# Kernel tuning notes

Hardware: AMD Instinct MI355X
Metric: run time of the kernel (lower is better)

The kernel has to match this reference:

```python
import jax, jax.numpy as jnp
import numpy as np

N, E, G = 16384, 131072, 64
IN_DIM, HID, HEADS, GDIM, OUT_DIM = 256, 128, 4, 2, 2


def _glorot(key, shape):
    fan_in = shape[0]
    return jax.random.normal(key, shape, dtype=jnp.float32) / jnp.sqrt(jnp.float32(fan_in))


def gatv2_layer(x, src, dst, Wl, bl, Wr, br, att, bias, heads, ch, concat):
    """GATv2Conv: e_ij = att . leaky_relu(Wl x_j + Wr x_i, 0.2), segment softmax over dst."""
    n = x.shape[0]
    xl = (x @ Wl + bl).reshape(n, heads, ch)  # source transform
    xr = (x @ Wr + br).reshape(n, heads, ch)  # target transform
    h = jax.nn.leaky_relu(xl[src] + xr[dst], 0.2)          # [E', H, C]
    e = jnp.einsum('ehc,hc->eh', h, att)                   # [E', H]
    m = jax.ops.segment_max(e, dst, num_segments=n)        # stable softmax per target
    p = jnp.exp(e - m[dst])
    denom = jax.ops.segment_sum(p, dst, num_segments=n)
    alpha = p / denom[dst]                                 # self-loops guarantee denom>0
    out = jax.ops.segment_sum(alpha[..., None] * xl[src], dst, num_segments=n)  # [n,H,C]
    out = out.reshape(n, heads * ch) if concat else out.mean(axis=1)
    return out + bias


def setup_inputs() -> dict:
    key = jax.random.key(0)
    ks = jax.random.split(key, 24)
    inp = {
        'x': jax.random.normal(ks[0], (N, IN_DIM), dtype=jnp.float32),
        'edge_index': jax.random.randint(ks[1], (2, E), 0, N, dtype=jnp.int64)
            if jax.config.jax_enable_x64 else jax.random.randint(ks[1], (2, E), 0, N).astype(jnp.int32),
        'batch': jnp.sort(jax.random.randint(ks[2], (N,), 0, G)).astype(jnp.int32),
        'global_features': jax.random.normal(ks[3], (G, GDIM), dtype=jnp.float32),
    }
    # conv1: in=256 -> heads*hid=512 (concat)
    inp['c1_Wl'] = _glorot(ks[4], (IN_DIM, HEADS * HID)); inp['c1_bl'] = jnp.zeros((HEADS * HID,), jnp.float32)
    inp['c1_Wr'] = _glorot(ks[5], (IN_DIM, HEADS * HID)); inp['c1_br'] = jnp.zeros((HEADS * HID,), jnp.float32)
    inp['c1_att'] = _glorot(ks[6], (HEADS, HID)); inp['c1_bias'] = jnp.zeros((HEADS * HID,), jnp.float32)
    # conv2: in=512 -> 512 (concat)
    D2 = HEADS * HID
    inp['c2_Wl'] = _glorot(ks[7], (D2, HEADS * HID)); inp['c2_bl'] = jnp.zeros((HEADS * HID,), jnp.float32)
    inp['c2_Wr'] = _glorot(ks[8], (D2, HEADS * HID)); inp['c2_br'] = jnp.zeros((HEADS * HID,), jnp.float32)
    inp['c2_att'] = _glorot(ks[9], (HEADS, HID)); inp['c2_bias'] = jnp.zeros((HEADS * HID,), jnp.float32)
    # conv3: in=512 -> 128 (heads=1, concat=False)
    inp['c3_Wl'] = _glorot(ks[10], (D2, HID)); inp['c3_bl'] = jnp.zeros((HID,), jnp.float32)
    inp['c3_Wr'] = _glorot(ks[11], (D2, HID)); inp['c3_br'] = jnp.zeros((HID,), jnp.float32)
    inp['c3_att'] = _glorot(ks[12], (1, HID)); inp['c3_bias'] = jnp.zeros((HID,), jnp.float32)
    # classifier: (hid + global_dim) -> hid -> out
    inp['cls_W1'] = _glorot(ks[13], (HID + GDIM, HID)); inp['cls_b1'] = jnp.zeros((HID,), jnp.float32)
    inp['cls_W2'] = _glorot(ks[14], (HID, OUT_DIM)); inp['cls_b2'] = jnp.zeros((OUT_DIM,), jnp.float32)
    return inp


def reference(x, edge_index, batch, global_features,
              c1_Wl, c1_bl, c1_Wr, c1_br, c1_att, c1_bias,
              c2_Wl, c2_bl, c2_Wr, c2_br, c2_att, c2_bias,
              c3_Wl, c3_bl, c3_Wr, c3_br, c3_att, c3_bias,
              cls_W1, cls_b1, cls_W2, cls_b2):
    n = x.shape[0]
    # PyG GATv2Conv add_self_loops=True default
    loop = jnp.arange(n, dtype=edge_index.dtype)
    src = jnp.concatenate([edge_index[0], loop])
    dst = jnp.concatenate([edge_index[1], loop])

    h = jax.nn.leaky_relu(gatv2_layer(x, src, dst, c1_Wl, c1_bl, c1_Wr, c1_br, c1_att, c1_bias, HEADS, HID, True), 0.01)
    h = jax.nn.leaky_relu(gatv2_layer(h, src, dst, c2_Wl, c2_bl, c2_Wr, c2_br, c2_att, c2_bias, HEADS, HID, True), 0.01)
    h = jax.nn.leaky_relu(gatv2_layer(h, src, dst, c3_Wl, c3_bl, c3_Wr, c3_br, c3_att, c3_bias, 1, HID, False), 0.01)

    # global mean pool over graphs
    counts = jax.ops.segment_sum(jnp.ones((n,), h.dtype), batch, num_segments=G)
    pooled = jax.ops.segment_sum(h, batch, num_segments=G) / jnp.maximum(counts, 1.0)[:, None]

    z = jnp.concatenate([pooled, global_features.reshape(G, -1)], axis=-1)
    z = jax.nn.leaky_relu(z @ cls_W1 + cls_b1, 0.01)  # Dropout is identity at eval
    return z @ cls_W2 + cls_b2
```

## Files before the change

### kernel.cpp

```cpp
#include <hip/hip_runtime.h>

typedef _Float16 h16;
typedef _Float16 h16x8 __attribute__((ext_vector_type(8)));
typedef float    f32x4 __attribute__((ext_vector_type(4)));

#define ELLW 40

__device__ __forceinline__ void gload16(const h16* g, h16* l) {
    __builtin_amdgcn_global_load_lds(
        (const __attribute__((address_space(1))) void*)g,
        (__attribute__((address_space(3))) void*)l,
        16, 0, 0);
}

__global__ __launch_bounds__(256) void prep(
    const float* __restrict__ W0, const float* __restrict__ W1,
    const float* __restrict__ W2, const float* __restrict__ W3,
    const float* __restrict__ W4, const float* __restrict__ W5,
    h16* __restrict__ O0, h16* __restrict__ O1, h16* __restrict__ O2,
    h16* __restrict__ O3, h16* __restrict__ O4, h16* __restrict__ O5,
    const float* __restrict__ x, h16* __restrict__ xh,
    int* __restrict__ cursor,
    const int* __restrict__ batch, int* __restrict__ start,
    float* __restrict__ pooled, int Nn, int G)
{
    __shared__ float lds[32][33];
    const int b = blockIdx.x;
    if (b < 896) {
        int mtx, t0;
        if      (b < 128) { mtx = 0; t0 = 0;   }
        else if (b < 256) { mtx = 1; t0 = 128; }
        else if (b < 512) { mtx = 2; t0 = 256; }
        else if (b < 768) { mtx = 3; t0 = 512; }
        else if (b < 832) { mtx = 4; t0 = 768; }
        else              { mtx = 5; t0 = 832; }
        const float* Ws[6] = {W0, W1, W2, W3, W4, W5};
        h16*         Os[6] = {O0, O1, O2, O3, O4, O5};
        const int    Ks[6] = {256, 256, 512, 512, 512, 512};
        const int    Ns[6] = {512, 512, 512, 512, 128, 128};
        const float* W = Ws[mtx];
        h16*         O = Os[mtx];
        const int K = Ks[mtx], N = Ns[mtx];
        const int tile = b - t0;
        const int tk = tile / (N >> 5), tn = tile % (N >> 5);
        const int t = threadIdx.x;
        const int r = t >> 3, c4 = (t & 7) * 4;
        float4 v = *(const float4*)(W + (size_t)(tk * 32 + r) * N + tn * 32 + c4);
        lds[r][c4] = v.x; lds[r][c4 + 1] = v.y; lds[r][c4 + 2] = v.z; lds[r][c4 + 3] = v.w;
        __syncthreads();
        h16* po = O + (size_t)(tn * 32 + r) * K + tk * 32 + c4;
        po[0] = (h16)lds[c4 + 0][r];
        po[1] = (h16)lds[c4 + 1][r];
        po[2] = (h16)lds[c4 + 2][r];
        po[3] = (h16)lds[c4 + 3][r];
        return;
    }
    int i = (b - 896) * 256 + threadIdx.x;
    const int n_x = Nn * 32;
    if (i < n_x) {
        float4 a = *(const float4*)(x + (size_t)i * 8);
        float4 c = *(const float4*)(x + (size_t)i * 8 + 4);
        h16x8 o = { (h16)a.x, (h16)a.y, (h16)a.z, (h16)a.w,
                    (h16)c.x, (h16)c.y, (h16)c.z, (h16)c.w };
        *(h16x8*)(xh + (size_t)i * 8) = o;
        return;
    }
    i -= n_x;
    if (i < Nn) { cursor[i] = 0; return; }
    i -= Nn;
    if (i < G * 128) { pooled[i] = 0.f; return; }
    i -= G * 128;
    if (i < Nn) {
        int bb = batch[i];
        int bp = (i == 0) ? -1 : batch[i - 1];
        for (int g = bp + 1; g <= bb; g++) start[g] = i;
        if (i == Nn - 1) for (int g = bb + 1; g <= G; g++) start[g] = Nn;
    }
}

__global__ void scatter_ell(const int* __restrict__ ei, int E, int Nn,
                            int* __restrict__ cursor, int* __restrict__ ssrc) {
    int i = blockIdx.x * blockDim.x + threadIdx.x;
    if (i >= E + Nn) return;
    int src, dst;
    if (i < E) { src = ei[i]; dst = ei[E + i]; }
    else       { src = dst = i - E; }
    int p = atomicAdd(&cursor[dst], 1);
    if (p < ELLW) ssrc[dst * ELLW + p] = src;
}

__device__ __forceinline__ void xcd_tiles(int& mt, int& nt) {
    int d = blockIdx.x + blockIdx.y * gridDim.x;
    int k = d & 7, j = d >> 3;
    mt = k * (gridDim.y >> 3) + j / gridDim.x;
    nt = j % gridDim.x;
}

__global__ __launch_bounds__(512) void gemm_f16_wide(
    const h16* __restrict__ Xh, const h16* __restrict__ Wt,
    const float* __restrict__ bias_lo, const float* __restrict__ bias_hi, int nsplit,
    h16* __restrict__ Yl, h16* __restrict__ Yr, int M, int N, int K)
{
    __shared__ __align__(16) h16 As[2][128 * 64];
    __shared__ __align__(16) h16 Bs[2][256 * 64];

    int mt, nt;
    xcd_tiles(mt, nt);
    const int m0 = mt * 128;
    const int n0 = nt * 256;
    const int t = threadIdx.x;
    const int lane = t & 63;
    const int wid = t >> 6;
    const int wr = wid >> 2;
    const int wc = wid & 3;

    f32x4 acc[4][4] = {};

    const int lr = lane >> 3;
    const int sl = lane & 7;

    #define STAGE(b, k0)                                                          \
        _Pragma("unroll")                                                         \
        for (int q = 0; q < 6; q++) {                                             \
            int rb = wid + 8 * q;                                                 \
            if (rb < 16) {                                                        \
                int r = rb * 8 + lr;                                              \
                int col = (sl ^ (r & 7)) << 3;                                    \
                gload16(Xh + (size_t)(m0 + r) * K + (k0) + col, &As[b][rb * 8 * 64]); \
            } else {                                                              \
                int c = (rb - 16) * 8 + lr;                                       \
                int col = (sl ^ (c & 7)) << 3;                                    \
                gload16(Wt + (size_t)(n0 + c) * K + (k0) + col, &Bs[b][(rb - 16) * 8 * 64]); \
            }                                                                     \
        }

    STAGE(0, 0)
    __syncthreads();

    const int nkb = K >> 6;
    int buf = 0;
    for (int kb = 0; kb < nkb; kb++) {
        if (kb + 1 < nkb) { STAGE(buf ^ 1, (kb + 1) << 6) }
        #pragma unroll
        for (int ks = 0; ks < 2; ks++) {
            h16x8 af[4], bf[4];
            #pragma unroll
            for (int i = 0; i < 4; i++) {
                int r  = wr * 64 + i * 16 + (lane & 15);
                int s2 = ks * 4 + (lane >> 4);
                af[i] = *(const h16x8*)(&As[buf][r * 64 + ((s2 ^ (r & 7)) << 3)]);
                int c  = wc * 64 + i * 16 + (lane & 15);
                bf[i] = *(const h16x8*)(&Bs[buf][c * 64 + ((s2 ^ (c & 7)) << 3)]);
            }
            #pragma unroll
            for (int i = 0; i < 4; i++)
                #pragma unroll
                for (int j = 0; j < 4; j++)
                    acc[i][j] = __builtin_amdgcn_mfma_f32_16x16x32_f16(af[i], bf[j], acc[i][j], 0, 0, 0);
        }
        __syncthreads();
        buf ^= 1;
    }
    #undef STAGE

    const int crow = (lane >> 4) * 4;
    const int ccol = lane & 15;
    #pragma unroll
    for (int i = 0; i < 4; i++) {
        int rg = m0 + wr * 64 + i * 16 + crow;
        #pragma unroll
        for (int j = 0; j < 4; j++) {
            int cg = n0 + wc * 64 + j * 16 + ccol;
            float b = (cg < nsplit) ? bias_lo[cg] : bias_hi[cg - nsplit];
            h16* dst = (cg < nsplit) ? (Yl + (size_t)cg) : (Yr + (size_t)(cg - nsplit));
            #pragma unroll
            for (int rr = 0; rr < 4; rr++)
                dst[(size_t)(rg + rr) * nsplit] = (h16)(acc[i][j][rr] + b);
        }
    }
}

__global__ __launch_bounds__(256) void gemm_f16_mfma(
    const h16* __restrict__ Xh, const h16* __restrict__ Wt,
    const float* __restrict__ bias_lo, const float* __restrict__ bias_hi, int nsplit,
    h16* __restrict__ Yl, h16* __restrict__ Yr, int M, int N, int K)
{
    __shared__ __align__(16) h16 As[2][128 * 64];
    __shared__ __align__(16) h16 Bs[2][128 * 64];

    int mt, nt;
    xcd_tiles(mt, nt);
    const int m0 = mt * 128;
    const int n0 = nt * 128;
    const int t = threadIdx.x;
    const int lane = t & 63;
    const int wid = t >> 6;
    const int wr = wid >> 1, wc = wid & 1;

    f32x4 acc[4][4] = {};

    const int rA = wid * 32;
    const int lr = lane >> 3;
    const int sl = lane & 7;

    #define STAGE(b, k0)                                                        \
        _Pragma("unroll")                                                       \
        for (int q = 0; q < 4; q++) {                                           \
            int rb = rA + q * 8;                                                \
            int r  = rb + lr;                                                   \
            int col = (sl ^ (r & 7)) << 3;                                      \
            gload16(Xh + (size_t)(m0 + r) * K + (k0) + col, &As[b][rb * 64]);   \
            gload16(Wt + (size_t)(n0 + r) * K + (k0) + col, &Bs[b][rb * 64]);   \
        }

    STAGE(0, 0)
    __syncthreads();

    const int nkb = K >> 6;
    int buf = 0;
    for (int kb = 0; kb < nkb; kb++) {
        if (kb + 1 < nkb) { STAGE(buf ^ 1, (kb + 1) << 6) }
        #pragma unroll
        for (int ks = 0; ks < 2; ks++) {
            h16x8 af[4], bf[4];
            #pragma unroll
            for (int i = 0; i < 4; i++) {
                int r  = wr * 64 + i * 16 + (lane & 15);
                int s2 = ks * 4 + (lane >> 4);
                af[i] = *(const h16x8*)(&As[buf][r * 64 + ((s2 ^ (r & 7)) << 3)]);
                int c  = wc * 64 + i * 16 + (lane & 15);
                bf[i] = *(const h16x8*)(&Bs[buf][c * 64 + ((s2 ^ (c & 7)) << 3)]);
            }
            #pragma unroll
            for (int i = 0; i < 4; i++)
                #pragma unroll
                for (int j = 0; j < 4; j++)
                    acc[i][j] = __builtin_amdgcn_mfma_f32_16x16x32_f16(af[i], bf[j], acc[i][j], 0, 0, 0);
        }
        __syncthreads();
        buf ^= 1;
    }
    #undef STAGE

    const int crow = (lane >> 4) * 4;
    const int ccol = lane & 15;
    #pragma unroll
    for (int i = 0; i < 4; i++) {
        int rg = m0 + wr * 64 + i * 16 + crow;
        #pragma unroll
        for (int j = 0; j < 4; j++) {
            int cg = n0 + wc * 64 + j * 16 + ccol;
            float b = (cg < nsplit) ? bias_lo[cg] : bias_hi[cg - nsplit];
            h16* dst = (cg < nsplit) ? (Yl + (size_t)cg) : (Yr + (size_t)(cg - nsplit));
            #pragma unroll
            for (int rr = 0; rr < 4; rr++)
                dst[(size_t)(rg + rr) * nsplit] = (h16)(acc[i][j][rr] + b);
        }
    }
}

template<int H, int C>
__global__ __launch_bounds__(256) void node_attn(
    const h16* __restrict__ xl, const h16* __restrict__ xr,
    const float* __restrict__ att, const float* __restrict__ bias,
    const int* __restrict__ deg, const int* __restrict__ ssrc,
    h16* __restrict__ out, int Nn)
{
    constexpr int D   = H * C;
    constexpr int EPL = D / 64;
    constexpr int LPH = C / EPL;
    int node = blockIdx.x * (blockDim.x >> 6) + (threadIdx.x >> 6);
    if (node >= Nn) return;
    const int lane = threadIdx.x & 63;
    const int base = lane * EPL;

    float xrv[EPL], attv[EPL];
    {
        h16x8 v = *(const h16x8*)(xr + (size_t)node * D + base);
        float4 a0 = *(const float4*)(att + base);
        float4 a1 = *(const float4*)(att + base + 4);
        #pragma unroll
        for (int j = 0; j < 8; j++) xrv[j] = (float)v[j];
        attv[0] = a0.x; attv[1] = a0.y; attv[2] = a0.z; attv[3] = a0.w;
        attv[4] = a1.x; attv[5] = a1.y; attv[6] = a1.z; attv[7] = a1.w;
    }

    float m = -INFINITY, denom = 0.f;
    float agg[EPL] = {};

    auto loadrow = [&](int src, float* xv) {
        h16x8 v = *(const h16x8*)(xl + (size_t)src * D + base);
        #pragma unroll
        for (int j = 0; j < 8; j++) xv[j] = (float)v[j];
    };
    auto score = [&](const float* xv) {
        float s = 0.f;
        #pragma unroll
        for (int j = 0; j < EPL; j++) {
            float v = xv[j] + xrv[j];
            v = v > 0.f ? v : 0.2f * v;
            s += v * attv[j];
        }
        return s;
    };
    auto update = [&](float s, const float* xv) {
        if (s > m) {
            float scale = __expf(m - s);
            denom *= scale;
            #pragma unroll
            for (int j = 0; j < EPL; j++) agg[j] *= scale;
            m = s;
        }
        float p = __expf(s - m);
        denom += p;
        #pragma unroll
        for (int j = 0; j < EPL; j++) agg[j] += p * xv[j];
    };

    const int e0 = node * ELLW, e1 = e0 + deg[node];
    int e = e0;
    for (; e + 7 < e1; e += 8) {
        int s[8];
        float xv[8][8], sc[8];
        #pragma unroll
        for (int g = 0; g < 8; g++) s[g] = ssrc[e + g];
        #pragma unroll
        for (int g = 0; g < 8; g++) loadrow(s[g], xv[g]);
        #pragma unroll
        for (int g = 0; g < 8; g++) sc[g] = score(xv[g]);
        #pragma unroll
        for (int o = 1; o < LPH; o <<= 1)
            #pragma unroll
            for (int g = 0; g < 8; g++) sc[g] += __shfl_xor(sc[g], o, 64);
        #pragma unroll
        for (int g = 0; g < 8; g++) update(sc[g], xv[g]);
    }
    for (; e + 3 < e1; e += 4) {
        int s[4];
        float xv[4][8], sc[4];
        #pragma unroll
        for (int g = 0; g < 4; g++) s[g] = ssrc[e + g];
        #pragma unroll
        for (int g = 0; g < 4; g++) loadrow(s[g], xv[g]);
        #pragma unroll
        for (int g = 0; g < 4; g++) sc[g] = score(xv[g]);
        #pragma unroll
        for (int o = 1; o < LPH; o <<= 1)
            #pragma unroll
            for (int g = 0; g < 4; g++) sc[g] += __shfl_xor(sc[g], o, 64);
        #pragma unroll
        for (int g = 0; g < 4; g++) update(sc[g], xv[g]);
    }
    for (; e < e1; e++) {
        int s0 = ssrc[e];
        float xa[8];
        loadrow(s0, xa);
        float sc0 = score(xa);
        #pragma unroll
        for (int o = 1; o < LPH; o <<= 1) sc0 += __shfl_xor(sc0, o, 64);
        update(sc0, xa);
    }

    h16* po = out + (size_t)node * D + base;
    h16x8 o8;
    #pragma unroll
    for (int j = 0; j < 8; j++) {
        float v = agg[j] / denom + bias[base + j];
        o8[j] = (h16)(v > 0.f ? v : 0.01f * v);
    }
    *(h16x8*)po = o8;
}

__global__ __launch_bounds__(256) void node_attn_h1(
    const h16* __restrict__ xl, const h16* __restrict__ xr,
    const float* __restrict__ att, const float* __restrict__ bias,
    const int* __restrict__ deg, const int* __restrict__ ssrc,
    float* __restrict__ out, int Nn)
{
    int node = blockIdx.x * 4 + (threadIdx.x >> 6);
    if (node >= Nn) return;
    const int lane = threadIdx.x & 63;
    const int q    = lane >> 4;
    const int sl   = lane & 15;
    const int base = sl * 8;

    float xrv[8], attv[8];
    {
        h16x8 v = *(const h16x8*)(xr + (size_t)node * 128 + base);
        float4 a0 = *(const float4*)(att + base);
        float4 a1 = *(const float4*)(att + base + 4);
        #pragma unroll
        for (int j = 0; j < 8; j++) xrv[j] = (float)v[j];
        attv[0] = a0.x; attv[1] = a0.y; attv[2] = a0.z; attv[3] = a0.w;
        attv[4] = a1.x; attv[5] = a1.y; attv[6] = a1.z; attv[7] = a1.w;
    }

    float m = -1e30f, denom = 0.f;
    float agg[8] = {};

    const int e0 = node * ELLW, e1 = e0 + deg[node];
    for (int e = e0 + q; e < e1; e += 4) {
        int src = ssrc[e];
        h16x8 v = *(const h16x8*)(xl + (size_t)src * 128 + base);
        float xv[8];
        #pragma unroll
        for (int j = 0; j < 8; j++) xv[j] = (float)v[j];
        float s = 0.f;
        #pragma unroll
        for (int j = 0; j < 8; j++) {
            float u = xv[j] + xrv[j];
            u = u > 0.f ? u : 0.2f * u;
            s += u * attv[j];
        }
        #pragma unroll
        for (int o = 1; o < 16; o <<= 1) s += __shfl_xor(s, o, 64);
        if (s > m) {
            float sc = __expf(m - s);
            denom *= sc;
            #pragma unroll
            for (int j = 0; j < 8; j++) agg[j] *= sc;
            m = s;
        }
        float p = __expf(s - m);
        denom += p;
        #pragma unroll
        for (int j = 0; j < 8; j++) agg[j] += p * xv[j];
    }

    #pragma unroll
    for (int o = 16; o <= 32; o <<= 1) {
        float m2 = __shfl_xor(m, o, 64);
        float d2 = __shfl_xor(denom, o, 64);
        float a2[8];
        #pragma unroll
        for (int j = 0; j < 8; j++) a2[j] = __shfl_xor(agg[j], o, 64);
        float mn = fmaxf(m, m2);
        float sa = __expf(m - mn), sb = __expf(m2 - mn);
        denom = denom * sa + d2 * sb;
        #pragma unroll
        for (int j = 0; j < 8; j++) agg[j] = agg[j] * sa + a2[j] * sb;
        m = mn;
    }

    if (lane < 16) {
        float* po = out + (size_t)node * 128 + base;
        #pragma unroll
        for (int j = 0; j < 8; j++) {
            float v = agg[j] / denom + bias[base + j];
            po[j] = v > 0.f ? v : 0.01f * v;
        }
    }
}

__global__ __launch_bounds__(128) void pool_partial(
    const float* __restrict__ h, const int* __restrict__ batch,
    float* __restrict__ pooled, int Nn, int spb)
{
    int t = threadIdx.x;
    int n0 = blockIdx.x * spb;
    int n1 = min(n0 + spb, Nn);
    if (n0 >= n1) return;
    int cur = batch[n0];
    float acc = 0.f;
    for (int n = n0; n < n1; n++) {
        int g = batch[n];
        if (g != cur) {
            atomicAdd(&pooled[cur * 128 + t], acc);
            acc = 0.f; cur = g;
        }
        acc += h[(size_t)n * 128 + t];
    }
    atomicAdd(&pooled[cur * 128 + t], acc);
}

__global__ __launch_bounds__(128) void classifier(
    const float* __restrict__ pooled, const int* __restrict__ start,
    const float* __restrict__ gf,
    const float* __restrict__ W1, const float* __restrict__ b1,
    const float* __restrict__ W2, const float* __restrict__ b2,
    float* __restrict__ out)
{
    __shared__ float z[130];
    __shared__ float hid[128];
    int g = blockIdx.x, t = threadIdx.x;
    float cnt = fmaxf((float)(start[g + 1] - start[g]), 1.f);
    z[t] = pooled[g * 128 + t] / cnt;
    if (t < 2) z[128 + t] = gf[g * 2 + t];
    __syncthreads();
    float s = b1[t];
    for (int k = 0; k < 130; k++) s += z[k] * W1[k * 128 + t];
    hid[t] = s > 0.f ? s : 0.01f * s;
    __syncthreads();
    if (t < 2) {
        float o = b2[t];
        for (int j = 0; j < 128; j++) o += hid[j] * W2[j * 2 + t];
        out[g * 2 + t] = o;
    }
}

static inline int cdiv(int a, int b) { return (a + b - 1) / b; }

extern "C" void kernel_launch(void* const* d_in, const int* in_sizes, int n_in,
                              void* d_out, int out_size, void* d_ws, size_t ws_size,
                              hipStream_t stream)
{
    const float* x     = (const float*)d_in[0];
    const int*   ei    = (const int*)d_in[1];
    const int*   batch = (const int*)d_in[2];
    const float* gf    = (const float*)d_in[3];

    const float* c_Wl[3]   = {(const float*)d_in[4],  (const float*)d_in[10], (const float*)d_in[16]};
    const float* c_bl[3]   = {(const float*)d_in[5],  (const float*)d_in[11], (const float*)d_in[17]};
    const float* c_Wr[3]   = {(const float*)d_in[6],  (const float*)d_in[12], (const float*)d_in[18]};
    const float* c_br[3]   = {(const float*)d_in[7],  (const float*)d_in[13], (const float*)d_in[19]};
    const float* c_att[3]  = {(const float*)d_in[8],  (const float*)d_in[14], (const float*)d_in[20]};
    const float* c_bias[3] = {(const float*)d_in[9],  (const float*)d_in[15], (const float*)d_in[21]};
    const float* W1 = (const float*)d_in[22];
    const float* b1 = (const float*)d_in[23];
    const float* W2 = (const float*)d_in[24];
    const float* b2 = (const float*)d_in[25];
    float* out = (float*)d_out;

    const int Nn   = in_sizes[0] / 256;
    const int E    = in_sizes[1] / 2;
    const int G    = in_sizes[3] / 2;
    const int Etot = E + Nn;

    char* w = (char*)d_ws;
    auto carve = [&](size_t bytes) { void* p = w; w += (bytes + 255) & ~(size_t)255; return p; };
    h16*   ylb  = (h16*)carve((size_t)Nn * 512 * 2);
    h16*   yrb  = (h16*)carve((size_t)Nn * 512 * 2);
    h16*   xh   = (h16*)carve((size_t)Nn * 512 * 2);
    float* b0   = (float*)carve((size_t)Nn * 128 * 4);
    h16* wt1 = (h16*)carve((size_t)1024 * 256 * 2);
    h16* wt2 = (h16*)carve((size_t)1024 * 512 * 2);
    h16* wt3 = (h16*)carve((size_t)256 * 512 * 2);
    int* cursor = (int*)carve((size_t)Nn * 4);
    int* ssrc   = (int*)carve((size_t)Nn * ELLW * 4);
    int* start  = (int*)carve((size_t)(G + 1) * 4);
    float* pooled = (float*)carve((size_t)G * 128 * 4);
    (void)ws_size; (void)n_in; (void)out_size;

    {
        const int flat = Nn * 32 + Nn + G * 128 + Nn;
        prep<<<896 + cdiv(flat, 256), 256, 0, stream>>>(
            c_Wl[0], c_Wr[0], c_Wl[1], c_Wr[1], c_Wl[2], c_Wr[2],
            wt1, wt1 + 512 * 256, wt2, wt2 + 512 * 512, wt3, wt3 + 128 * 512,
            x, xh, cursor, batch, start, pooled, Nn, G);
    }
    scatter_ell<<<cdiv(Etot, 256), 256, 0, stream>>>(ei, E, Nn, cursor, ssrc);

    const int node_blocks = cdiv(Nn, 4);

    gemm_f16_wide<<<dim3(1024 / 256, Nn / 128), 512, 0, stream>>>(xh, wt1, c_bl[0], c_br[0], 512, ylb, yrb, Nn, 1024, 256);
    node_attn<4, 128><<<node_blocks, 256, 0, stream>>>(ylb, yrb, c_att[0], c_bias[0], cursor, ssrc, xh, Nn);
    gemm_f16_wide<<<dim3(1024 / 256, Nn / 128), 512, 0, stream>>>(xh, wt2, c_bl[1], c_br[1], 512, ylb, yrb, Nn, 1024, 512);
    node_attn<4, 128><<<node_blocks, 256, 0, stream>>>(ylb, yrb, c_att[1], c_bias[1], cursor, ssrc, xh, Nn);
    gemm_f16_mfma<<<dim3(256 / 128, Nn / 128), 256, 0, stream>>>(xh, wt3, c_bl[2], c_br[2], 128, ylb, yrb, Nn, 256, 512);
    node_attn_h1<<<node_blocks, 256, 0, stream>>>(ylb, yrb, c_att[2], c_bias[2], cursor, ssrc, b0, Nn);

    {
        const int nblk = 256;
        const int spb  = cdiv(Nn, nblk);
        pool_partial<<<nblk, 128, 0, stream>>>(b0, batch, pooled, Nn, spb);
    }
    classifier<<<G, 128, 0, stream>>>(pooled, start, gf, W1, b1, W2, b2, out);
}
```

Before: 193.4 us.

## Fuse mean pooling into classifier and keep gathered rows as packed fp16

After: 239.8 us. +24.0%, slower.

```diff
diff --git a/kernel.cpp b/kernel.cpp
--- a/kernel.cpp
+++ b/kernel.cpp
@@ -22,7 +22,7 @@
     const float* __restrict__ x, h16* __restrict__ xh,
     int* __restrict__ cursor,
     const int* __restrict__ batch, int* __restrict__ start,
-    float* __restrict__ pooled, int Nn, int G)
+    int Nn, int G)
 {
     __shared__ float lds[32][33];
     const int b = blockIdx.x;
@@ -68,8 +68,6 @@
     i -= n_x;
     if (i < Nn) { cursor[i] = 0; return; }
     i -= Nn;
-    if (i < G * 128) { pooled[i] = 0.f; return; }
-    i -= G * 128;
     if (i < Nn) {
         int bb = batch[i];
         int bp = (i == 0) ? -1 : batch[i - 1];
@@ -260,7 +258,7 @@
 }
 
 template<int H, int C>
-__global__ __launch_bounds__(256) void node_attn(
+__global__ __launch_bounds__(256, 5) void node_attn(
     const h16* __restrict__ xl, const h16* __restrict__ xr,
     const float* __restrict__ att, const float* __restrict__ bias,
     const int* __restrict__ deg, const int* __restrict__ ssrc,
@@ -288,77 +286,73 @@
     float m = -INFINITY, denom = 0.f;
     float agg[EPL] = {};
 
-    auto loadrow = [&](int src, float* xv) {
-        h16x8 v = *(const h16x8*)(xl + (size_t)src * D + base);
-        #pragma unroll
-        for (int j = 0; j < 8; j++) xv[j] = (float)v[j];
-    };
-    auto score = [&](const float* xv) {
+    auto score8 = [&](h16x8 v) {
         float s = 0.f;
         #pragma unroll
-        for (int j = 0; j < EPL; j++) {
-            float v = xv[j] + xrv[j];
-            v = v > 0.f ? v : 0.2f * v;
-            s += v * attv[j];
+        for (int j = 0; j < 8; j++) {
+            float u = (float)v[j] + xrv[j];
+            u = u > 0.f ? u : 0.2f * u;
+            s += u * attv[j];
         }
         return s;
     };
-    auto update = [&](float s, const float* xv) {
+    auto update8 = [&](float s, h16x8 v) {
         if (s > m) {
             float scale = __expf(m - s);
             denom *= scale;
             #pragma unroll
-            for (int j = 0; j < EPL; j++) agg[j] *= scale;
+            for (int j = 0; j < 8; j++) agg[j] *= scale;
             m = s;
         }
         float p = __expf(s - m);
         denom += p;
         #pragma unroll
-        for (int j = 0; j < EPL; j++) agg[j] += p * xv[j];
+        for (int j = 0; j < 8; j++) agg[j] += p * (float)v[j];
     };
 
     const int e0 = node * ELLW, e1 = e0 + deg[node];
     int e = e0;
     for (; e + 7 < e1; e += 8) {
         int s[8];
-        float xv[8][8], sc[8];
+        h16x8 xv[8];
+        float sc[8];
         #pragma unroll
         for (int g = 0; g < 8; g++) s[g] = ssrc[e + g];
         #pragma unroll
-        for (int g = 0; g < 8; g++) loadrow(s[g], xv[g]);
-        #pragma unroll
-        for (int g = 0; g < 8; g++) sc[g] = score(xv[g]);
+        for (int g = 0; g < 8; g++) xv[g] = *(const h16x8*)(xl + (size_t)s[g] * D + base);
+        #pragma unroll
+        for (int g = 0; g < 8; g++) sc[g] = score8(xv[g]);
         #pragma unroll
         for (int o = 1; o < LPH; o <<= 1)
             #pragma unroll
             for (int g = 0; g < 8; g++) sc[g] += __shfl_xor(sc[g], o, 64);
         #pragma unroll
-        for (int g = 0; g < 8; g++) update(sc[g], xv[g]);
+        for (int g = 0; g < 8; g++) update8(sc[g], xv[g]);
     }
     for (; e + 3 < e1; e += 4) {
         int s[4];
-        float xv[4][8], sc[4];
+        h16x8 xv[4];
+        float sc[4];
         #pragma unroll
         for (int g = 0; g < 4; g++) s[g] = ssrc[e + g];
         #pragma unroll
-        for (int g = 0; g < 4; g++) loadrow(s[g], xv[g]);
-        #pragma unroll
-        for (int g = 0; g < 4; g++) sc[g] = score(xv[g]);
+        for (int g = 0; g < 4; g++) xv[g] = *(const h16x8*)(xl + (size_t)s[g] * D + base);
+        #pragma unroll
+        for (int g = 0; g < 4; g++) sc[g] = score8(xv[g]);
         #pragma unroll
         for (int o = 1; o < LPH; o <<= 1)
             #pragma unroll
             for (int g = 0; g < 4; g++) sc[g] += __shfl_xor(sc[g], o, 64);
         #pragma unroll
-        for (int g = 0; g < 4; g++) update(sc[g], xv[g]);
+        for (int g = 0; g < 4; g++) update8(sc[g], xv[g]);
     }
     for (; e < e1; e++) {
         int s0 = ssrc[e];
-        float xa[8];
-        loadrow(s0, xa);
-        float sc0 = score(xa);
+        h16x8 xa = *(const h16x8*)(xl + (size_t)s0 * D + base);
+        float sc0 = score8(xa);
         #pragma unroll
         for (int o = 1; o < LPH; o <<= 1) sc0 += __shfl_xor(sc0, o, 64);
-        update(sc0, xa);
+        update8(sc0, xa);
     }
 
     h16* po = out + (size_t)node * D + base;
@@ -402,13 +396,10 @@
     for (int e = e0 + q; e < e1; e += 4) {
         int src = ssrc[e];
         h16x8 v = *(const h16x8*)(xl + (size_t)src * 128 + base);
-        float xv[8];
-        #pragma unroll
-        for (int j = 0; j < 8; j++) xv[j] = (float)v[j];
         float s = 0.f;
         #pragma unroll
         for (int j = 0; j < 8; j++) {
-            float u = xv[j] + xrv[j];
+            float u = (float)v[j] + xrv[j];
             u = u > 0.f ? u : 0.2f * u;
             s += u * attv[j];
         }
@@ -424,7 +415,7 @@
         float p = __expf(s - m);
         denom += p;
         #pragma unroll
-        for (int j = 0; j < 8; j++) agg[j] += p * xv[j];
+        for (int j = 0; j < 8; j++) agg[j] += p * (float)v[j];
     }
 
     #pragma unroll
@@ -452,44 +443,35 @@
     }
 }
 
-__global__ __launch_bounds__(128) void pool_partial(
-    const float* __restrict__ h, const int* __restrict__ batch,
-    float* __restrict__ pooled, int Nn, int spb)
-{
-    int t = threadIdx.x;
-    int n0 = blockIdx.x * spb;
-    int n1 = min(n0 + spb, Nn);
-    if (n0 >= n1) return;
-    int cur = batch[n0];
-    float acc = 0.f;
-    for (int n = n0; n < n1; n++) {
-        int g = batch[n];
-        if (g != cur) {
-            atomicAdd(&pooled[cur * 128 + t], acc);
-            acc = 0.f; cur = g;
-        }
-        acc += h[(size_t)n * 128 + t];
-    }
-    atomicAdd(&pooled[cur * 128 + t], acc);
-}
-
-__global__ __launch_bounds__(128) void classifier(
-    const float* __restrict__ pooled, const int* __restrict__ start,
+__global__ __launch_bounds__(256) void pool_cls(
+    const float* __restrict__ b0, const int* __restrict__ start,
     const float* __restrict__ gf,
     const float* __restrict__ W1, const float* __restrict__ b1,
     const float* __restrict__ W2, const float* __restrict__ b2,
     float* __restrict__ out)
 {
-    __shared__ float z[130];
+    __shared__ float zz[130];
+    __shared__ float psum[128];
     __shared__ float hid[128];
-    int g = blockIdx.x, t = threadIdx.x;
-    float cnt = fmaxf((float)(start[g + 1] - start[g]), 1.f);
-    z[t] = pooled[g * 128 + t] / cnt;
-    if (t < 2) z[128 + t] = gf[g * 2 + t];
+    const int g = blockIdx.x, t = threadIdx.x;
+    const int s0 = start[g], s1 = start[g + 1];
+    const int ch = t & 127, half = t >> 7;
+
+    float acc = 0.f;
+    for (int n = s0 + half; n < s1; n += 2) acc += b0[(size_t)n * 128 + ch];
+    if (half) psum[ch] = acc;
     __syncthreads();
-    float s = b1[t];
-    for (int k = 0; k < 130; k++) s += z[k] * W1[k * 128 + t];
-    hid[t] = s > 0.f ? s : 0.01f * s;
+    if (!half) {
+        float tot = acc + psum[ch];
+        zz[ch] = tot / fmaxf((float)(s1 - s0), 1.f);
+        if (ch < 2) zz[128 + ch] = gf[g * 2 + ch];
+    }
+    __syncthreads();
+    if (t < 128) {
+        float s = b1[t];
+        for (int k = 0; k < 130; k++) s += zz[k] * W1[k * 128 + t];
+        hid[t] = s > 0.f ? s : 0.01f * s;
+    }
     __syncthreads();
     if (t < 2) {
         float o = b2[t];
@@ -538,15 +520,14 @@
     int* cursor = (int*)carve((size_t)Nn * 4);
     int* ssrc   = (int*)carve((size_t)Nn * ELLW * 4);
     int* start  = (int*)carve((size_t)(G + 1) * 4);
-    float* pooled = (float*)carve((size_t)G * 128 * 4);
     (void)ws_size; (void)n_in; (void)out_size;
 
     {
-        const int flat = Nn * 32 + Nn + G * 128 + Nn;
+        const int flat = Nn * 32 + Nn + Nn;
         prep<<<896 + cdiv(flat, 256), 256, 0, stream>>>(
             c_Wl[0], c_Wr[0], c_Wl[1], c_Wr[1], c_Wl[2], c_Wr[2],
             wt1, wt1 + 512 * 256, wt2, wt2 + 512 * 512, wt3, wt3 + 128 * 512,
-            x, xh, cursor, batch, start, pooled, Nn, G);
+            x, xh, cursor, batch, start, Nn, G);
     }
     scatter_ell<<<cdiv(Etot, 256), 256, 0, stream>>>(ei, E, Nn, cursor, ssrc);
 
@@ -559,10 +540,5 @@
     gemm_f16_mfma<<<dim3(256 / 128, Nn / 128), 256, 0, stream>>>(xh, wt3, c_bl[2], c_br[2], 128, ylb, yrb, Nn, 256, 512);
     node_attn_h1<<<node_blocks, 256, 0, stream>>>(ylb, yrb, c_att[2], c_bias[2], cursor, ssrc, b0, Nn);
 
-    {
-        const int nblk = 256;
-        const int spb  = cdiv(Nn, nblk);
-        pool_partial<<<nblk, 128, 0, stream>>>(b0, batch, pooled, Nn, spb);
-    }
-    classifier<<<G, 128, 0, stream>>>(pooled, start, gf, W1, b1, W2, b2, out);
-}
+    pool_cls<<<G, 256, 0, stream>>>(b0, start, gf, W1, b1, W2, b2, out);
+}
```
